# Performance work log

Measured on AMD Instinct MI355X. Metric: run time of the kernel, lower is better.

Reference implementation:

```python
import jax, jax.numpy as jnp
import numpy as np

D_MODEL = 1024
NHEAD = 16
HEAD_DIM = D_MODEL // NHEAD
EPS = 1e-5


def _layer_norm(x, gamma, beta):
    mu = jnp.mean(x, axis=-1, keepdims=True)
    var = jnp.mean(jnp.square(x - mu), axis=-1, keepdims=True)
    return (x - mu) * jax.lax.rsqrt(var + EPS) * gamma + beta


def setup_inputs() -> dict:
    key = jax.random.key(0)
    ks = jax.random.split(key, 8)
    s = 1.0 / np.sqrt(D_MODEL)
    return {
        "x": jax.random.normal(ks[0], (4, 2048, D_MODEL), dtype=jnp.float32),
        "Wq": jax.random.uniform(ks[1], (D_MODEL, D_MODEL), jnp.float32, -s, s),
        "Wk": jax.random.uniform(ks[2], (D_MODEL, D_MODEL), jnp.float32, -s, s),
        "Wv": jax.random.uniform(ks[3], (D_MODEL, D_MODEL), jnp.float32, -s, s),
        "ln1_g": jnp.ones((D_MODEL,), jnp.float32),
        "ln1_b": jnp.zeros((D_MODEL,), jnp.float32),
        "ln2_g": jnp.ones((D_MODEL,), jnp.float32),
        "ln2_b": jnp.zeros((D_MODEL,), jnp.float32),
        "W1": jax.random.uniform(ks[4], (D_MODEL, D_MODEL), jnp.float32, -s, s),
        "b1": jax.random.uniform(ks[5], (D_MODEL,), jnp.float32, -s, s),
        "W2": jax.random.uniform(ks[6], (D_MODEL, D_MODEL), jnp.float32, -s, s),
        "b2": jax.random.uniform(ks[7], (D_MODEL,), jnp.float32, -s, s),
    }


def reference(x, Wq, Wk, Wv, ln1_g, ln1_b, ln2_g, ln2_b, W1, b1, W2, b2):
    B, S, D = x.shape
    temperature = jnp.sqrt(jnp.asarray(D_MODEL / NHEAD, x.dtype))
    xn = _layer_norm(x, ln1_g, ln1_b)
    # torch Linear: y = x @ W.T (weights are [out, in], no bias for q/k/v)
    q = (xn @ Wq.T).reshape(B, S, NHEAD, HEAD_DIM)
    k = (xn @ Wk.T).reshape(B, S, NHEAD, HEAD_DIM)
    v = (xn @ Wv.T).reshape(B, S, NHEAD, HEAD_DIM)
    scores = jnp.einsum("bqhd,bkhd->bhqk", q, k) / temperature  # [B,H,S,S]
    causal = jnp.tril(jnp.ones((S, S), dtype=bool))
    scores = jnp.where(causal, scores, jnp.asarray(-jnp.inf, scores.dtype))
    attn = jax.nn.softmax(scores, axis=-1)
    att_out = jnp.einsum("bhqk,bkhd->bqhd", attn, v).reshape(B, S, D)
    xt = x + att_out
    xt2 = _layer_norm(xt, ln2_g, ln2_b)
    ffn = jax.nn.relu(xt2 @ W1.T + b1) @ W2.T + b2  # dropout=0 -> identity
    return xt + ffn
```

## Files before the change

### kernel.cpp

```cpp
#include <hip/hip_runtime.h>
#include <hip/hip_bf16.h>

typedef unsigned short u16;
typedef unsigned int u32;
typedef __attribute__((ext_vector_type(8))) __bf16 bf16x8;
typedef __attribute__((ext_vector_type(4))) float f32x4;
typedef __attribute__((ext_vector_type(8))) unsigned short ushort8v;
typedef __attribute__((ext_vector_type(4))) unsigned short u16x4;
typedef __attribute__((ext_vector_type(2))) unsigned int u32x2;

#define DEV __device__ __forceinline__
#define AS1 __attribute__((address_space(1)))
#define AS3 __attribute__((address_space(3)))

DEV u16 f2bf(float f) {
    union { float f; unsigned int i; } u; u.f = f;
    unsigned int x = u.i;
    unsigned int r = (x + 0x7fffu + ((x >> 16) & 1u)) >> 16;
    return (u16)r;
}
DEV float bf2f(u16 h) {
    union { unsigned int i; float f; } u; u.i = ((unsigned int)h) << 16;
    return u.f;
}
DEV u32 cvt_pk_bf16(float lo, float hi) {
    u32 r;
    asm("v_cvt_pk_bf16_f32 %0, %1, %2" : "=v"(r) : "v"(lo), "v"(hi));
    return r;
}

__global__ __launch_bounds__(256) void cvt_w(
    const float* __restrict__ wq, const float* __restrict__ wk,
    const float* __restrict__ wv, const float* __restrict__ w1,
    const float* __restrict__ w2, u16* __restrict__ dst)
{
    const int i = (blockIdx.x * 256 + threadIdx.x) * 4;
    if (i >= (1 << 20)) return;
    auto conv4 = [](float4 a) {
        u16x4 r; r[0] = f2bf(a.x); r[1] = f2bf(a.y); r[2] = f2bf(a.z); r[3] = f2bf(a.w);
        return r;
    };
    *(u16x4*)(dst + i)               = conv4(*(const float4*)(wq + i));
    *(u16x4*)(dst + (1 << 20) + i)   = conv4(*(const float4*)(wk + i));
    *(u16x4*)(dst + (2 << 20) + i)   = conv4(*(const float4*)(wv + i));
    *(u16x4*)(dst + (3 << 20) + i)   = conv4(*(const float4*)(w1 + i));
    *(u16x4*)(dst + (4 << 20) + i)   = conv4(*(const float4*)(w2 + i));
}

template<bool ADD>
__global__ __launch_bounds__(256) void ln_kernel(
    const float* __restrict__ xin, const u16* __restrict__ addbf,
    const float* __restrict__ g, const float* __restrict__ be,
    float* __restrict__ xt_out, u16* __restrict__ y_bf)
{
    const int row = blockIdx.x;
    const int tid = threadIdx.x;
    const size_t base = (size_t)row * 1024 + tid * 4;

    float4 xv = *(const float4*)(xin + base);
    float v[4] = {xv.x, xv.y, xv.z, xv.w};
    if (ADD) {
        u16x4 a = *(const u16x4*)(addbf + base);
        v[0] += bf2f(a[0]); v[1] += bf2f(a[1]); v[2] += bf2f(a[2]); v[3] += bf2f(a[3]);
        float4 o; o.x = v[0]; o.y = v[1]; o.z = v[2]; o.w = v[3];
        *(float4*)(xt_out + base) = o;
    }
    float s = 0.f, ss = 0.f;
    #pragma unroll
    for (int j = 0; j < 4; ++j) { s += v[j]; ss += v[j] * v[j]; }
    #pragma unroll
    for (int o = 32; o > 0; o >>= 1) { s += __shfl_xor(s, o); ss += __shfl_xor(ss, o); }
    __shared__ float red[8];
    const int w = tid >> 6;
    if ((tid & 63) == 0) { red[w * 2] = s; red[w * 2 + 1] = ss; }
    __syncthreads();
    s  = red[0] + red[2] + red[4] + red[6];
    ss = red[1] + red[3] + red[5] + red[7];
    const float mu = s * (1.0f / 1024.0f);
    const float var = ss * (1.0f / 1024.0f) - mu * mu;
    const float rstd = rsqrtf(var + 1e-5f);

    const int col = tid * 4;
    float4 gv = *(const float4*)(g + col);
    float4 bv = *(const float4*)(be + col);
    u16x4 o4;
    o4[0] = f2bf((v[0] - mu) * rstd * gv.x + bv.x);
    o4[1] = f2bf((v[1] - mu) * rstd * gv.y + bv.y);
    o4[2] = f2bf((v[2] - mu) * rstd * gv.z + bv.z);
    o4[3] = f2bf((v[3] - mu) * rstd * gv.w + bv.w);
    *(u16x4*)(y_bf + base) = o4;
}

template<int EPI>
__global__ __launch_bounds__(256, 2) void gemm_bt(
    const u16* __restrict__ A, const u16* __restrict__ Bt,
    void* __restrict__ Cout, const float* __restrict__ bias,
    const float* __restrict__ resid, int M, int N, int K)
{
    __shared__ u16 As[2][2 * 128 * 32];
    __shared__ u16 Bs[2][2 * 128 * 32];
    const int tid = threadIdx.x;
    const int l = tid & 63;
    const int w = tid >> 6;
    const int wm = w >> 1, wn = w & 1;
    const int fr = l & 15, fc = l >> 4;
    const size_t rowA0 = (size_t)blockIdx.x * 128;
    const size_t rowB0 = (size_t)blockIdx.y * 128;

    f32x4 acc[4][4] = {};
    const int ldoff = fr * 32 + fc * 8;

    const int srow = (l >> 2);
    const int skk  = (l & 3) * 8;

    auto STAGE = [&](int kt, int p) {
        const int k0 = kt << 6;
        #pragma unroll
        for (int q = 0; q < 4; ++q) {
            const int row = (q & 1) * 64 + w * 16 + srow;
            const int kk  = (q >> 1) * 32 + skk;
            const u16* ga = A  + (rowA0 + row) * K + k0 + kk;
            const u16* gb = Bt + (rowB0 + row) * K + k0 + kk;
            __builtin_amdgcn_global_load_lds((const AS1 void*)ga,
                (AS3 void*)(&As[p][0] + q * 2048 + w * 512), 16, 0, 0);
            __builtin_amdgcn_global_load_lds((const AS1 void*)gb,
                (AS3 void*)(&Bs[p][0] + q * 2048 + w * 512), 16, 0, 0);
        }
    };

    const int nkt = K >> 6;
    STAGE(0, 0);
    asm volatile("s_waitcnt vmcnt(0)" ::: "memory");
    __builtin_amdgcn_s_barrier();

    for (int kt = 0; kt < nkt; ++kt) {
        const int p = kt & 1;
        if (kt + 1 < nkt) STAGE(kt + 1, p ^ 1);
        __builtin_amdgcn_sched_barrier(0);
        #pragma unroll
        for (int ks = 0; ks < 2; ++ks) {
            const u16* as_p = &As[p][0] + ks * 4096;
            const u16* bs_p = &Bs[p][0] + ks * 4096;
            bf16x8 af[4], bfv[4];
            #pragma unroll
            for (int m = 0; m < 4; ++m)
                af[m] = *(const bf16x8*)(as_p + (wm * 64 + m * 16) * 32 + ldoff);
            #pragma unroll
            for (int n = 0; n < 4; ++n)
                bfv[n] = *(const bf16x8*)(bs_p + (wn * 64 + n * 16) * 32 + ldoff);
            __builtin_amdgcn_s_setprio(1);
            #pragma unroll
            for (int m = 0; m < 4; ++m)
                #pragma unroll
                for (int n = 0; n < 4; ++n)
                    acc[m][n] = __builtin_amdgcn_mfma_f32_16x16x32_bf16(
                        af[m], bfv[n], acc[m][n], 0, 0, 0);
            __builtin_amdgcn_s_setprio(0);
        }
        if (kt + 1 < nkt) asm volatile("s_waitcnt vmcnt(0)" ::: "memory");
        asm volatile("s_waitcnt lgkmcnt(0)" ::: "memory");
        __builtin_amdgcn_s_barrier();
    }

    const int r0 = (int)rowA0 + wm * 64;
    const int c0 = (int)rowB0 + wn * 64;
    #pragma unroll
    for (int m = 0; m < 4; ++m) {
        #pragma unroll
        for (int n = 0; n < 4; ++n) {
            const int row = r0 + m * 16 + fc * 4;
            const int col = c0 + n * 16 + fr;
            #pragma unroll
            for (int j = 0; j < 4; ++j) {
                float v = acc[m][n][j];
                if constexpr (EPI == 0) {
                    const int rowj = row + j;
                    const int which = col >> 10;
                    const int hh = (col >> 6) & 15;
                    const int dd = col & 63;
                    const size_t dst = (size_t)which * 8388608 +
                        ((((size_t)(rowj >> 11) * 16 + hh) * 2048 + (rowj & 2047)) * 64 + dd);
                    ((u16*)Cout)[dst] = f2bf(v);
                } else if constexpr (EPI == 1) {
                    const size_t idx = (size_t)(row + j) * N + col;
                    v += bias[col];
                    v = fmaxf(v, 0.0f);
                    ((u16*)Cout)[idx] = f2bf(v);
                } else {
                    const size_t idx = (size_t)(row + j) * N + col;
                    v += bias[col] + resid[idx];
                    ((float*)Cout)[idx] = v;
                }
            }
        }
    }
}

__global__ __launch_bounds__(256, 4) void attn_fwd(
    const u16* __restrict__ Qh, const u16* __restrict__ Kh,
    const u16* __restrict__ Vh, u16* __restrict__ attout)
{
    __shared__ u16 Ks[2][64 * 64];
    __shared__ u16 Vt[2][64 * 64];
    __shared__ u16 Pw[4][16 * 64];

    const int bid = blockIdx.x;
    const int qt = (int)((0x32104567BA98CDEFull >> (((bid >> 6) & 15) * 4)) & 15);
    const int g = bid & 63;
    const int h = g & 15, b = g >> 4;

    const int tid = threadIdx.x, l = tid & 63, w = tid >> 6;
    const int fr = l & 15, fc = l >> 4;
    const int hb = b * 16 + h;
    const size_t head = (size_t)hb << 17;
    const u16* kb_g = Kh + head;
    const u16* vb_g = Vh + head;
    u16* pw = &Pw[w][0];

    const int sw = (fr & 7) << 3;
    const int col0 = (fc * 8) ^ sw;
    const int col1 = col0 ^ 32;

    const int krow0 = w * 16 + (l >> 3);
    const int kdsw  = ((l & 7) * 8) ^ ((l >> 3) << 3);

    const int kr = tid >> 2;
    const int kc0 = (tid & 3) * 16;

    const float qs = 0.125f * 1.44269504f;

    bf16x8 onesv;
    #pragma unroll
    for (int j = 0; j < 8; ++j) onesv[j] = (__bf16)1.0f;

    const int qbw = qt * 128 + w * 32;

    bf16x8 qf[2][2];
    #pragma unroll
    for (int qq = 0; qq < 2; ++qq) {
        const u16* qp = Qh + head + (size_t)(qbw + qq * 16 + fr) * 64 + fc * 8;
        qf[qq][0] = *(const bf16x8*)qp;
        qf[qq][1] = *(const bf16x8*)(qp + 32);
        #pragma unroll
        for (int j = 0; j < 8; ++j) {
            qf[qq][0][j] = (__bf16)((float)qf[qq][0][j] * qs);
            qf[qq][1][j] = (__bf16)((float)qf[qq][1][j] * qs);
        }
    }

    f32x4 acc_o[2][4] = {};
    f32x4 l_run[2] = {};
    float m_run[2] = {-3.0e38f, -3.0e38f};

    const int nkt = 2 * qt + 2;
    int cur = 0;

    #pragma unroll
    for (int i = 0; i < 2; ++i) {
        const int row = krow0 + i * 8;
        __builtin_amdgcn_global_load_lds(
            (const AS1 void*)(kb_g + (size_t)row * 64 + kdsw),
            (AS3 void*)(&Ks[0][0] + (w * 16 + i * 8) * 64), 16, 0, 0);
    }
    __builtin_amdgcn_sched_barrier(0);
    {
        ushort8v v0a = *(const ushort8v*)(vb_g + (size_t)kr * 64 + kc0);
        ushort8v v0b = *(const ushort8v*)(vb_g + (size_t)kr * 64 + kc0 + 8);
        #pragma unroll
        for (int j = 0; j < 8; ++j) {
            const int d0 = kc0 + j, d1 = kc0 + 8 + j;
            Vt[0][d0 * 64 + (kr ^ ((d0 & 7) << 3) ^ ((d0 >> 4) << 4))] = v0a[j];
            Vt[0][d1 * 64 + (kr ^ ((d1 & 7) << 3) ^ ((d1 >> 4) << 4))] = v0b[j];
        }
    }
    ushort8v vA, vB;
    vA = *(const ushort8v*)(vb_g + (size_t)(64 + kr) * 64 + kc0);
    vB = *(const ushort8v*)(vb_g + (size_t)(64 + kr) * 64 + kc0 + 8);
    __builtin_amdgcn_sched_barrier(0);
    asm volatile("s_waitcnt vmcnt(2)" ::: "memory");
    asm volatile("s_waitcnt lgkmcnt(0)" ::: "memory");
    __builtin_amdgcn_s_barrier();

    #pragma unroll 1
    for (int kt = 0; kt < nkt; ++kt) {
        const int kv0 = kt * 64;
        const u16* ksc = &Ks[cur][0];
        const u16* vtc = &Vt[cur][0];

        if (kt + 1 < nkt) {
            u16* ksn = &Ks[cur ^ 1][0];
            #pragma unroll
            for (int i = 0; i < 2; ++i) {
                const int row = krow0 + i * 8;
                __builtin_amdgcn_global_load_lds(
                    (const AS1 void*)(kb_g + (size_t)(kv0 + 64 + row) * 64 + kdsw),
                    (AS3 void*)(ksn + (w * 16 + i * 8) * 64), 16, 0, 0);
            }
        }
        __builtin_amdgcn_sched_barrier(0);

        if (kv0 <= qbw + 31) {
            f32x4 sa[2][4] = {};
            __builtin_amdgcn_s_setprio(1);
            #pragma unroll
            for (int nb = 0; nb < 4; ++nb) {
                const u16* kb = ksc + (nb * 16 + fr) * 64;
                const bf16x8 kf0 = *(const bf16x8*)(kb + col0);
                const bf16x8 kf1 = *(const bf16x8*)(kb + col1);
                #pragma unroll
                for (int qq = 0; qq < 2; ++qq) {
                    sa[qq][nb] = __builtin_amdgcn_mfma_f32_16x16x32_bf16(
                        kf0, qf[qq][0], sa[qq][nb], 0, 0, 0);
                    sa[qq][nb] = __builtin_amdgcn_mfma_f32_16x16x32_bf16(
                        kf1, qf[qq][1], sa[qq][nb], 0, 0, 0);
                }
            }
            __builtin_amdgcn_s_setprio(0);

            if (kv0 + 64 > qbw) {
                #pragma unroll
                for (int qq = 0; qq < 2; ++qq) {
                    const int qg = qbw + qq * 16 + fr;
                    #pragma unroll
                    for (int nb = 0; nb < 4; ++nb)
                        #pragma unroll
                        for (int j = 0; j < 4; ++j) {
                            const int kg = kv0 + nb * 16 + fc * 4 + j;
                            if (kg > qg) sa[qq][nb][j] = -3.0e38f;
                        }
                }
            }

            float mx[2];
            #pragma unroll
            for (int qq = 0; qq < 2; ++qq) {
                float m = sa[qq][0][0];
                #pragma unroll
                for (int nb = 0; nb < 4; ++nb)
                    #pragma unroll
                    for (int j = 0; j < 4; ++j)
                        m = fmaxf(m, sa[qq][nb][j]);
                m = fmaxf(m, __shfl_xor(m, 16));
                m = fmaxf(m, __shfl_xor(m, 32));
                mx[qq] = m;
            }

            const bool need = (mx[0] > m_run[0] + 8.0f) || (mx[1] > m_run[1] + 8.0f);
            if (__any(need)) {
                #pragma unroll
                for (int qq = 0; qq < 2; ++qq) {
                    const float mn = fmaxf(m_run[qq], mx[qq]);
                    const float alpha = exp2f(m_run[qq] - mn);
                    m_run[qq] = mn;
                    #pragma unroll
                    for (int j = 0; j < 4; ++j) {
                        const float aj = __shfl(alpha, fc * 4 + j);
                        l_run[qq][j] *= aj;
                        #pragma unroll
                        for (int db = 0; db < 4; ++db)
                            acc_o[qq][db][j] *= aj;
                    }
                }
            }

            #pragma unroll
            for (int qq = 0; qq < 2; ++qq)
                #pragma unroll
                for (int nb = 0; nb < 4; ++nb)
                    #pragma unroll
                    for (int j = 0; j < 4; ++j)
                        sa[qq][nb][j] = exp2f(sa[qq][nb][j] - m_run[qq]);

            bf16x8 pf[2][2];
            #pragma unroll
            for (int qq = 0; qq < 2; ++qq) {
                #pragma unroll
                for (int nb = 0; nb < 4; ++nb) {
                    u32x2 pkv;
                    pkv[0] = cvt_pk_bf16(sa[qq][nb][0], sa[qq][nb][1]);
                    pkv[1] = cvt_pk_bf16(sa[qq][nb][2], sa[qq][nb][3]);
                    *(u32x2*)(pw + fr * 64 + ((nb * 16 + fc * 4) ^ sw)) = pkv;
                }
                const u16* prd = pw + fr * 64;
                pf[qq][0] = *(const bf16x8*)(prd + col0);
                pf[qq][1] = *(const bf16x8*)(prd + col1);
            }
            f32x4 acc_s[2] = {};
            __builtin_amdgcn_s_setprio(1);
            #pragma unroll
            for (int db = 0; db < 4; ++db) {
                const u16* vb = vtc + (db * 16 + fr) * 64;
                const int vx = db << 4;
                const bf16x8 vf0 = *(const bf16x8*)(vb + (col0 ^ vx));
                const bf16x8 vf1 = *(const bf16x8*)(vb + (col1 ^ vx));
                #pragma unroll
                for (int qq = 0; qq < 2; ++qq) {
                    acc_o[qq][db] = __builtin_amdgcn_mfma_f32_16x16x32_bf16(
                        pf[qq][0], vf0, acc_o[qq][db], 0, 0, 0);
                    acc_o[qq][db] = __builtin_amdgcn_mfma_f32_16x16x32_bf16(
                        pf[qq][1], vf1, acc_o[qq][db], 0, 0, 0);
                }
            }
            #pragma unroll
            for (int qq = 0; qq < 2; ++qq) {
                acc_s[qq] = __builtin_amdgcn_mfma_f32_16x16x32_bf16(
                    pf[qq][0], onesv, acc_s[qq], 0, 0, 0);
                acc_s[qq] = __builtin_amdgcn_mfma_f32_16x16x32_bf16(
                    pf[qq][1], onesv, acc_s[qq], 0, 0, 0);
            }
            __builtin_amdgcn_s_setprio(0);
            #pragma unroll
            for (int qq = 0; qq < 2; ++qq)
                #pragma unroll
                for (int j = 0; j < 4; ++j)
                    l_run[qq][j] += acc_s[qq][j];
        }

        if (kt + 1 < nkt) {
            u16* vtn = &Vt[cur ^ 1][0];
            #pragma unroll
            for (int j = 0; j < 8; ++j) {
                const int d0 = kc0 + j, d1 = kc0 + 8 + j;
                vtn[d0 * 64 + (kr ^ ((d0 & 7) << 3) ^ ((d0 >> 4) << 4))] = vA[j];
                vtn[d1 * 64 + (kr ^ ((d1 & 7) << 3) ^ ((d1 >> 4) << 4))] = vB[j];
            }
        }
        if (kt + 2 < nkt) {
            const u16* vn = vb_g + (size_t)(kv0 + 128 + kr) * 64 + kc0;
            vA = *(const ushort8v*)vn;
            vB = *(const ushort8v*)(vn + 8);
        }
        __builtin_amdgcn_sched_barrier(0);
        if (kt + 1 < nkt) {
            if (kt + 2 < nkt) asm volatile("s_waitcnt vmcnt(2)" ::: "memory");
            else              asm volatile("s_waitcnt vmcnt(0)" ::: "memory");
        }
        asm volatile("s_waitcnt lgkmcnt(0)" ::: "memory");
        __builtin_amdgcn_s_barrier();
        cur ^= 1;
    }

    const size_t bS = (size_t)b * 2048;
    #pragma unroll
    for (int qq = 0; qq < 2; ++qq) {
        float inv[4];
        #pragma unroll
        for (int j = 0; j < 4; ++j) inv[j] = 1.0f / l_run[qq][j];
        #pragma unroll
        for (int db = 0; db < 4; ++db)
            #pragma unroll
            for (int j = 0; j < 4; ++j)
                attout[(bS + qbw + qq * 16 + fc * 4 + j) * 1024 + h * 64 + db * 16 + fr] =
                    f2bf(acc_o[qq][db][j] * inv[j]);
    }
}

extern "C" void kernel_launch(void* const* d_in, const int* in_sizes, int n_in,
                              void* d_out, int out_size, void* d_ws, size_t ws_size,
                              hipStream_t stream)
{
    const float* x    = (const float*)d_in[0];
    const float* Wq   = (const float*)d_in[1];
    const float* Wk   = (const float*)d_in[2];
    const float* Wv   = (const float*)d_in[3];
    const float* ln1g = (const float*)d_in[4];
    const float* ln1b = (const float*)d_in[5];
    const float* ln2g = (const float*)d_in[6];
    const float* ln2b = (const float*)d_in[7];
    const float* W1   = (const float*)d_in[8];
    const float* b1   = (const float*)d_in[9];
    const float* W2   = (const float*)d_in[10];
    const float* b2   = (const float*)d_in[11];

    char* ws = (char*)d_ws;
    u16*   wbf  = (u16*)(ws);
    u16*   xn   = (u16*)(ws + 10485760);
    u16*   qkvb = (u16*)(ws + 27262976);
    u16*   attb = (u16*)(ws + 77594624);
    float* xt   = (float*)(ws + 94371840);

    cvt_w<<<1024, 256, 0, stream>>>(Wq, Wk, Wv, W1, W2, wbf);
    ln_kernel<false><<<8192, 256, 0, stream>>>(x, nullptr, ln1g, ln1b, nullptr, xn);
    gemm_bt<0><<<dim3(64, 24), 256, 0, stream>>>(xn, wbf, qkvb, nullptr, nullptr,
                                                 8192, 3072, 1024);
    attn_fwd<<<1024, 256, 0, stream>>>(qkvb, qkvb + 8388608, qkvb + 16777216, attb);
    ln_kernel<true><<<8192, 256, 0, stream>>>(x, attb, ln2g, ln2b, xt, xn);
    gemm_bt<1><<<dim3(64, 8), 256, 0, stream>>>(xn, wbf + (3 << 20), qkvb, b1, nullptr,
                                                8192, 1024, 1024);
    gemm_bt<2><<<dim3(64, 8), 256, 0, stream>>>(qkvb, wbf + (4 << 20), d_out, b2, xt,
                                                8192, 1024, 1024);
}
```

Measured before the change: 258.8 us.

## Pair mirrored query tiles in attention and store residual in bf16

Each attention block now handles two 64-row query tiles, tile p and tile 31-p, so that every block has a near-equal causal workload of 32-p key tiles. The second tile is always active and the first tile's MFMA work is gated by a per-iteration predicate. This replaces the earlier 128-row tiles whose cost varied widely across blocks. Separately, the residual xt is stored as bf16 rather than fp32, which halves that buffer's write and read traffic in the LN2 and FFN2 epilogue at some cost in precision.

```diff
diff --git a/kernel.cpp b/kernel.cpp
--- a/kernel.cpp
+++ b/kernel.cpp
@@ -51,7 +51,7 @@
 __global__ __launch_bounds__(256) void ln_kernel(
     const float* __restrict__ xin, const u16* __restrict__ addbf,
     const float* __restrict__ g, const float* __restrict__ be,
-    float* __restrict__ xt_out, u16* __restrict__ y_bf)
+    u16* __restrict__ xt_out, u16* __restrict__ y_bf)
 {
     const int row = blockIdx.x;
     const int tid = threadIdx.x;
@@ -62,8 +62,9 @@
     if (ADD) {
         u16x4 a = *(const u16x4*)(addbf + base);
         v[0] += bf2f(a[0]); v[1] += bf2f(a[1]); v[2] += bf2f(a[2]); v[3] += bf2f(a[3]);
-        float4 o; o.x = v[0]; o.y = v[1]; o.z = v[2]; o.w = v[3];
-        *(float4*)(xt_out + base) = o;
+        u16x4 o;
+        o[0] = f2bf(v[0]); o[1] = f2bf(v[1]); o[2] = f2bf(v[2]); o[3] = f2bf(v[3]);
+        *(u16x4*)(xt_out + base) = o;
     }
     float s = 0.f, ss = 0.f;
     #pragma unroll
@@ -95,7 +96,7 @@
 __global__ __launch_bounds__(256, 2) void gemm_bt(
     const u16* __restrict__ A, const u16* __restrict__ Bt,
     void* __restrict__ Cout, const float* __restrict__ bias,
-    const float* __restrict__ resid, int M, int N, int K)
+    const u16* __restrict__ resid, int M, int N, int K)
 {
     __shared__ u16 As[2][2 * 128 * 32];
     __shared__ u16 Bs[2][2 * 128 * 32];
@@ -188,7 +189,7 @@
                     ((u16*)Cout)[idx] = f2bf(v);
                 } else {
                     const size_t idx = (size_t)(row + j) * N + col;
-                    v += bias[col] + resid[idx];
+                    v += bias[col] + bf2f(resid[idx]);
                     ((float*)Cout)[idx] = v;
                 }
             }
@@ -205,7 +206,7 @@
     __shared__ u16 Pw[4][16 * 64];
 
     const int bid = blockIdx.x;
-    const int qt = (int)((0x32104567BA98CDEFull >> (((bid >> 6) & 15) * 4)) & 15);
+    const int p = (int)((0x32104567BA98CDEFull >> (((bid >> 6) & 15) * 4)) & 15);
     const int g = bid & 63;
     const int h = g & 15, b = g >> 4;
 
@@ -233,12 +234,12 @@
     #pragma unroll
     for (int j = 0; j < 8; ++j) onesv[j] = (__bf16)1.0f;
 
-    const int qbw = qt * 128 + w * 32;
+    const int qb[2] = { p * 64 + w * 16, (31 - p) * 64 + w * 16 };
 
     bf16x8 qf[2][2];
     #pragma unroll
     for (int qq = 0; qq < 2; ++qq) {
-        const u16* qp = Qh + head + (size_t)(qbw + qq * 16 + fr) * 64 + fc * 8;
+        const u16* qp = Qh + head + (size_t)(qb[qq] + fr) * 64 + fc * 8;
         qf[qq][0] = *(const bf16x8*)qp;
         qf[qq][1] = *(const bf16x8*)(qp + 32);
         #pragma unroll
@@ -252,7 +253,7 @@
     f32x4 l_run[2] = {};
     float m_run[2] = {-3.0e38f, -3.0e38f};
 
-    const int nkt = 2 * qt + 2;
+    const int nkt = 32 - p;
     int cur = 0;
 
     #pragma unroll
@@ -286,6 +287,7 @@
         const int kv0 = kt * 64;
         const u16* ksc = &Ks[cur][0];
         const u16* vtc = &Vt[cur][0];
+        const bool act0 = (kt <= p);
 
         if (kt + 1 < nkt) {
             u16* ksn = &Ks[cur ^ 1][0];
@@ -299,121 +301,138 @@
         }
         __builtin_amdgcn_sched_barrier(0);
 
-        if (kv0 <= qbw + 31) {
-            f32x4 sa[2][4] = {};
-            __builtin_amdgcn_s_setprio(1);
-            #pragma unroll
-            for (int nb = 0; nb < 4; ++nb) {
-                const u16* kb = ksc + (nb * 16 + fr) * 64;
-                const bf16x8 kf0 = *(const bf16x8*)(kb + col0);
-                const bf16x8 kf1 = *(const bf16x8*)(kb + col1);
+        f32x4 sa[2][4] = {};
+        __builtin_amdgcn_s_setprio(1);
+        #pragma unroll
+        for (int nb = 0; nb < 4; ++nb) {
+            const u16* kb = ksc + (nb * 16 + fr) * 64;
+            const bf16x8 kf0 = *(const bf16x8*)(kb + col0);
+            const bf16x8 kf1 = *(const bf16x8*)(kb + col1);
+            sa[1][nb] = __builtin_amdgcn_mfma_f32_16x16x32_bf16(
+                kf0, qf[1][0], sa[1][nb], 0, 0, 0);
+            sa[1][nb] = __builtin_amdgcn_mfma_f32_16x16x32_bf16(
+                kf1, qf[1][1], sa[1][nb], 0, 0, 0);
+            if (act0) {
+                sa[0][nb] = __builtin_amdgcn_mfma_f32_16x16x32_bf16(
+                    kf0, qf[0][0], sa[0][nb], 0, 0, 0);
+                sa[0][nb] = __builtin_amdgcn_mfma_f32_16x16x32_bf16(
+                    kf1, qf[0][1], sa[0][nb], 0, 0, 0);
+            }
+        }
+        __builtin_amdgcn_s_setprio(0);
+
+        if (kt == p) {
+            const int qg = qb[0] + fr;
+            #pragma unroll
+            for (int nb = 0; nb < 4; ++nb)
                 #pragma unroll
-                for (int qq = 0; qq < 2; ++qq) {
-                    sa[qq][nb] = __builtin_amdgcn_mfma_f32_16x16x32_bf16(
-                        kf0, qf[qq][0], sa[qq][nb], 0, 0, 0);
-                    sa[qq][nb] = __builtin_amdgcn_mfma_f32_16x16x32_bf16(
-                        kf1, qf[qq][1], sa[qq][nb], 0, 0, 0);
+                for (int j = 0; j < 4; ++j) {
+                    const int kg = kv0 + nb * 16 + fc * 4 + j;
+                    if (kg > qg) sa[0][nb][j] = -3.0e38f;
                 }
-            }
-            __builtin_amdgcn_s_setprio(0);
-
-            if (kv0 + 64 > qbw) {
+        }
+        if (kt == nkt - 1) {
+            const int qg = qb[1] + fr;
+            #pragma unroll
+            for (int nb = 0; nb < 4; ++nb)
                 #pragma unroll
-                for (int qq = 0; qq < 2; ++qq) {
-                    const int qg = qbw + qq * 16 + fr;
-                    #pragma unroll
-                    for (int nb = 0; nb < 4; ++nb)
-                        #pragma unroll
-                        for (int j = 0; j < 4; ++j) {
-                            const int kg = kv0 + nb * 16 + fc * 4 + j;
-                            if (kg > qg) sa[qq][nb][j] = -3.0e38f;
-                        }
+                for (int j = 0; j < 4; ++j) {
+                    const int kg = kv0 + nb * 16 + fc * 4 + j;
+                    if (kg > qg) sa[1][nb][j] = -3.0e38f;
                 }
-            }
-
-            float mx[2];
-            #pragma unroll
-            for (int qq = 0; qq < 2; ++qq) {
-                float m = sa[qq][0][0];
-                #pragma unroll
-                for (int nb = 0; nb < 4; ++nb)
-                    #pragma unroll
-                    for (int j = 0; j < 4; ++j)
-                        m = fmaxf(m, sa[qq][nb][j]);
-                m = fmaxf(m, __shfl_xor(m, 16));
-                m = fmaxf(m, __shfl_xor(m, 32));
-                mx[qq] = m;
-            }
-
-            const bool need = (mx[0] > m_run[0] + 8.0f) || (mx[1] > m_run[1] + 8.0f);
-            if (__any(need)) {
-                #pragma unroll
-                for (int qq = 0; qq < 2; ++qq) {
-                    const float mn = fmaxf(m_run[qq], mx[qq]);
-                    const float alpha = exp2f(m_run[qq] - mn);
-                    m_run[qq] = mn;
-                    #pragma unroll
-                    for (int j = 0; j < 4; ++j) {
-                        const float aj = __shfl(alpha, fc * 4 + j);
-                        l_run[qq][j] *= aj;
-                        #pragma unroll
-                        for (int db = 0; db < 4; ++db)
-                            acc_o[qq][db][j] *= aj;
-                    }
-                }
-            }
-
-            #pragma unroll
-            for (int qq = 0; qq < 2; ++qq)
-                #pragma unroll
-                for (int nb = 0; nb < 4; ++nb)
-                    #pragma unroll
-                    for (int j = 0; j < 4; ++j)
-                        sa[qq][nb][j] = exp2f(sa[qq][nb][j] - m_run[qq]);
-
-            bf16x8 pf[2][2];
-            #pragma unroll
-            for (int qq = 0; qq < 2; ++qq) {
-                #pragma unroll
-                for (int nb = 0; nb < 4; ++nb) {
-                    u32x2 pkv;
-                    pkv[0] = cvt_pk_bf16(sa[qq][nb][0], sa[qq][nb][1]);
-                    pkv[1] = cvt_pk_bf16(sa[qq][nb][2], sa[qq][nb][3]);
-                    *(u32x2*)(pw + fr * 64 + ((nb * 16 + fc * 4) ^ sw)) = pkv;
-                }
-                const u16* prd = pw + fr * 64;
-                pf[qq][0] = *(const bf16x8*)(prd + col0);
-                pf[qq][1] = *(const bf16x8*)(prd + col1);
-            }
-            f32x4 acc_s[2] = {};
-            __builtin_amdgcn_s_setprio(1);
-            #pragma unroll
-            for (int db = 0; db < 4; ++db) {
-                const u16* vb = vtc + (db * 16 + fr) * 64;
-                const int vx = db << 4;
-                const bf16x8 vf0 = *(const bf16x8*)(vb + (col0 ^ vx));
-                const bf16x8 vf1 = *(const bf16x8*)(vb + (col1 ^ vx));
-                #pragma unroll
-                for (int qq = 0; qq < 2; ++qq) {
-                    acc_o[qq][db] = __builtin_amdgcn_mfma_f32_16x16x32_bf16(
-                        pf[qq][0], vf0, acc_o[qq][db], 0, 0, 0);
-                    acc_o[qq][db] = __builtin_amdgcn_mfma_f32_16x16x32_bf16(
-                        pf[qq][1], vf1, acc_o[qq][db], 0, 0, 0);
-                }
-            }
-            #pragma unroll
-            for (int qq = 0; qq < 2; ++qq) {
-                acc_s[qq] = __builtin_amdgcn_mfma_f32_16x16x32_bf16(
-                    pf[qq][0], onesv, acc_s[qq], 0, 0, 0);
-                acc_s[qq] = __builtin_amdgcn_mfma_f32_16x16x32_bf16(
-                    pf[qq][1], onesv, acc_s[qq], 0, 0, 0);
-            }
-            __builtin_amdgcn_s_setprio(0);
-            #pragma unroll
-            for (int qq = 0; qq < 2; ++qq)
+        }
+
+        const int qlo = act0 ? 0 : 1;
+        float mx[2];
+        #pragma unroll
+        for (int qq = 0; qq < 2; ++qq) {
+            if (qq < qlo) continue;
+            float m = sa[qq][0][0];
+            #pragma unroll
+            for (int nb = 0; nb < 4; ++nb)
                 #pragma unroll
                 for (int j = 0; j < 4; ++j)
-                    l_run[qq][j] += acc_s[qq][j];
+                    m = fmaxf(m, sa[qq][nb][j]);
+            m = fmaxf(m, __shfl_xor(m, 16));
+            m = fmaxf(m, __shfl_xor(m, 32));
+            mx[qq] = m;
+        }
+
+        bool need = (mx[1] > m_run[1] + 8.0f);
+        if (act0) need = need || (mx[0] > m_run[0] + 8.0f);
+        if (__any(need)) {
+            #pragma unroll
+            for (int qq = 0; qq < 2; ++qq) {
+                if (qq < qlo) continue;
+                const float mn = fmaxf(m_run[qq], mx[qq]);
+                const float alpha = exp2f(m_run[qq] - mn);
+                m_run[qq] = mn;
+                #pragma unroll
+                for (int j = 0; j < 4; ++j) {
+                    const float aj = __shfl(alpha, fc * 4 + j);
+                    l_run[qq][j] *= aj;
+                    #pragma unroll
+                    for (int db = 0; db < 4; ++db)
+                        acc_o[qq][db][j] *= aj;
+                }
+            }
+        }
+
+        #pragma unroll
+        for (int qq = 0; qq < 2; ++qq) {
+            if (qq < qlo) continue;
+            #pragma unroll
+            for (int nb = 0; nb < 4; ++nb)
+                #pragma unroll
+                for (int j = 0; j < 4; ++j)
+                    sa[qq][nb][j] = exp2f(sa[qq][nb][j] - m_run[qq]);
+        }
+
+        bf16x8 pf[2][2];
+        #pragma unroll
+        for (int qq = 0; qq < 2; ++qq) {
+            if (qq < qlo) continue;
+            #pragma unroll
+            for (int nb = 0; nb < 4; ++nb) {
+                u32x2 pkv;
+                pkv[0] = cvt_pk_bf16(sa[qq][nb][0], sa[qq][nb][1]);
+                pkv[1] = cvt_pk_bf16(sa[qq][nb][2], sa[qq][nb][3]);
+                *(u32x2*)(pw + fr * 64 + ((nb * 16 + fc * 4) ^ sw)) = pkv;
+            }
+            const u16* prd = pw + fr * 64;
+            pf[qq][0] = *(const bf16x8*)(prd + col0);
+            pf[qq][1] = *(const bf16x8*)(prd + col1);
+        }
+        f32x4 acc_s[2] = {};
+        __builtin_amdgcn_s_setprio(1);
+        #pragma unroll
+        for (int db = 0; db < 4; ++db) {
+            const u16* vb = vtc + (db * 16 + fr) * 64;
+            const int vx = db << 4;
+            const bf16x8 vf0 = *(const bf16x8*)(vb + (col0 ^ vx));
+            const bf16x8 vf1 = *(const bf16x8*)(vb + (col1 ^ vx));
+            acc_o[1][db] = __builtin_amdgcn_mfma_f32_16x16x32_bf16(
+                pf[1][0], vf0, acc_o[1][db], 0, 0, 0);
+            acc_o[1][db] = __builtin_amdgcn_mfma_f32_16x16x32_bf16(
+                pf[1][1], vf1, acc_o[1][db], 0, 0, 0);
+            if (act0) {
+                acc_o[0][db] = __builtin_amdgcn_mfma_f32_16x16x32_bf16(
+                    pf[0][0], vf0, acc_o[0][db], 0, 0, 0);
+                acc_o[0][db] = __builtin_amdgcn_mfma_f32_16x16x32_bf16(
+                    pf[0][1], vf1, acc_o[0][db], 0, 0, 0);
+            }
+        }
+        acc_s[1] = __builtin_amdgcn_mfma_f32_16x16x32_bf16(pf[1][0], onesv, acc_s[1], 0, 0, 0);
+        acc_s[1] = __builtin_amdgcn_mfma_f32_16x16x32_bf16(pf[1][1], onesv, acc_s[1], 0, 0, 0);
+        if (act0) {
+            acc_s[0] = __builtin_amdgcn_mfma_f32_16x16x32_bf16(pf[0][0], onesv, acc_s[0], 0, 0, 0);
+            acc_s[0] = __builtin_amdgcn_mfma_f32_16x16x32_bf16(pf[0][1], onesv, acc_s[0], 0, 0, 0);
+        }
+        __builtin_amdgcn_s_setprio(0);
+        #pragma unroll
+        for (int j = 0; j < 4; ++j) {
+            l_run[1][j] += acc_s[1][j];
+            if (act0) l_run[0][j] += acc_s[0][j];
         }
 
         if (kt + 1 < nkt) {
@@ -450,7 +469,7 @@
         for (int db = 0; db < 4; ++db)
             #pragma unroll
             for (int j = 0; j < 4; ++j)
-                attout[(bS + qbw + qq * 16 + fc * 4 + j) * 1024 + h * 64 + db * 16 + fr] =
+                attout[(bS + qb[qq] + fc * 4 + j) * 1024 + h * 64 + db * 16 + fr] =
                     f2bf(acc_o[qq][db][j] * inv[j]);
     }
 }
@@ -477,7 +496,7 @@
     u16*   xn   = (u16*)(ws + 10485760);
     u16*   qkvb = (u16*)(ws + 27262976);
     u16*   attb = (u16*)(ws + 77594624);
-    float* xt   = (float*)(ws + 94371840);
+    u16*   xt   = (u16*)(ws + 94371840);
 
     cvt_w<<<1024, 256, 0, stream>>>(Wq, Wk, Wv, W1, W2, wbf);
     ln_kernel<false><<<8192, 256, 0, stream>>>(x, nullptr, ln1g, ln1b, nullptr, xn);
```

After: 297.4 us. 14.9% more time.
